# Kernel tuning notes

Hardware: AMD Instinct MI355X
Metric: run time of the kernel (lower is better)

## Reference

```python
import jax, jax.numpy as jnp
import numpy as np

B, V, S = 16, 100000, 4096
LOSS_WEIGHT = 1.0


def setup_inputs() -> dict:
    key = jax.random.key(0)
    k1, k2, k3, k4 = jax.random.split(key, 4)
    return {
        "src_verts": jax.random.normal(k1, (B, V, 3), dtype=jnp.float32),
        "dst_verts": jax.random.normal(k2, (B, V, 3), dtype=jnp.float32),
        "src_idx": jax.random.randint(k3, (B, S), 0, V, dtype=jnp.int64),
        "dst_idx": jax.random.randint(k4, (B, S), 0, V, dtype=jnp.int64),
    }


def _gather(verts, idx):
    # verts: (B, V, 3), idx: (B, S) -> (B, S, 3)
    return jnp.take_along_axis(verts, idx[:, :, None], axis=1)


def reference(src_verts, dst_verts, src_idx, dst_idx):
    src = _gather(src_verts, src_idx)  # (B, S, 3)
    dst = _gather(dst_verts, dst_idx)  # (B, S, 3)
    # squared euclidean distance matrix, matching torch.cdist(p=2)**2
    s2 = jnp.sum(src * src, axis=-1)  # (B, S)
    d2 = jnp.sum(dst * dst, axis=-1)  # (B, S)
    gram = jnp.einsum("bsc,btc->bst", src, dst)  # (B, S, S)
    dist_mat = jnp.maximum(s2[:, :, None] + d2[:, None, :] - 2.0 * gram, 0.0)
    # min over src points (dim=1) + min over dst points (dim=2)
    chamfer_distance = jnp.min(dist_mat, axis=1) + jnp.min(dist_mat, axis=2)  # (B, S)
    chamfer_loss = jnp.mean(chamfer_distance, axis=-1)  # (B,)
    chamfer_loss = jnp.mean(chamfer_loss, axis=0)  # scalar ('mean' reduction)
    return chamfer_loss * LOSS_WEIGHT
```

## Files before the change

kernel.cpp:

```cpp
#include <hip/hip_runtime.h>
#include <hip/hip_bf16.h>
#include <math.h>

#define B 16
#define V 100000
#define S 4096
#define BS (B * S)
#define NT 256
#define ONE_BF 0x3F80u

typedef __attribute__((ext_vector_type(8))) short bf16x8;
typedef __attribute__((ext_vector_type(16))) float f32x16;

static __device__ __forceinline__ unsigned bft(float x) {
  return __float_as_uint(x) >> 16;
}
static __device__ __forceinline__ float bff(unsigned hbits) {
  return __uint_as_float(hbits << 16);
}
static __device__ __forceinline__ unsigned pk(unsigned lo, unsigned hi) {
  return (lo & 0xFFFFu) | (hi << 16);
}
static __device__ __forceinline__ float min3(float a, float b, float c) {
  return fminf(fminf(a, b), c);
}


__global__ __launch_bounds__(256) void chamfer_prep_kernel(
    const float* __restrict__ src_verts, const float* __restrict__ dst_verts,
    const int* __restrict__ src_idx, const int* __restrict__ dst_idx,
    uint4* __restrict__ srcfrag, uint4* __restrict__ dstfrag,
    float* __restrict__ out) {
  int t = blockIdx.x * 256 + threadIdx.x;
  if (t == 0) *out = 0.f;
  int set = t >> 16;
  int i = t & (BS - 1);
  int b = i >> 12;

  const int* idx = set ? dst_idx : src_idx;
  const float* verts = set ? dst_verts : src_verts;
  int v = idx[i];
  v = v < 0 ? 0 : (v >= V ? V - 1 : v);
  const float* pv = verts + ((size_t)b * V + v) * 3;
  float x = pv[0], y = pv[1], z = pv[2];
  unsigned hx = bft(x), hy = bft(y), hz = bft(z);
  float n2 = x * x + y * y + z * z;
  unsigned n2h = bft(n2);
  unsigned n2l = bft(n2 - bff(n2h));

  if (set == 0) {
    unsigned lx = bft(x - bff(hx)), ly = bft(y - bff(hy)), lz = bft(z - bff(hz));
    int tile = i >> 5, c = i & 31;
    uint4* base = srcfrag + (size_t)tile * 64;
    base[c]      = make_uint4(pk(hx, hy), pk(hz, lx), pk(ly, lz), pk(hx, hy));
    base[32 + c] = make_uint4(pk(hz, n2h), pk(n2l, ONE_BF), pk(ONE_BF, 0u), 0u);
  } else {
    unsigned mx = bft(-2.f * bff(hx)), my = bft(-2.f * bff(hy)), mz = bft(-2.f * bff(hz));
    unsigned nx = bft(-2.f * (x - bff(hx)));
    unsigned ny = bft(-2.f * (y - bff(hy)));
    unsigned nz = bft(-2.f * (z - bff(hz)));
    dstfrag[(size_t)i * 2]     = make_uint4(pk(mx, my), pk(mz, mx), pk(my, mz), pk(nx, ny));
    dstfrag[(size_t)i * 2 + 1] = make_uint4(pk(nz, ONE_BF), pk(ONE_BF, n2h), pk(n2l, 0u), 0u);
  }
}

__global__ __launch_bounds__(NT, 2) void chamfer_mfma_kernel(
    const uint4* __restrict__ srcfrag, const uint4* __restrict__ dstfrag,
    float* __restrict__ part_src, float* __restrict__ part_dst) {
  __shared__ struct {
    uint4 sfrag[2048];
    unsigned smin[1024];
  } sh;
  float* red = (float*)sh.sfrag;

  int bid = blockIdx.x;
  int b = bid >> 6;
  int jp = (bid >> 2) & 15;
  int iq = bid & 3;
  int tid = threadIdx.x;

  const uint4* chunk = srcfrag + (size_t)(b * 128 + iq * 32) * 64;
  #pragma unroll
  for (int k = 0; k < 8; ++k) {
    sh.sfrag[tid + k * NT] = chunk[tid + k * NT];
  }
  #pragma unroll
  for (int k = 0; k < 4; ++k) sh.smin[tid + k * NT] = 0x7F800000u;

  int w = tid >> 6;
  int lane = tid & 63;
  int c = lane & 31, h = lane >> 5;
  int gj = b * S + jp * 256 + w * 64 + c;
  bf16x8 A0 = __builtin_bit_cast(bf16x8, dstfrag[(size_t)gj * 2 + h]);
  bf16x8 A1 = __builtin_bit_cast(bf16x8, dstfrag[(size_t)(gj + 32) * 2 + h]);

  __syncthreads();

  f32x16 zero = {};
  f32x16 mn0, mn1;
  #pragma unroll
  for (int r = 0; r < 16; ++r) { mn0[r] = INFINITY; mn1[r] = INFINITY; }

  int t0r = 8 * w;

  #define FOLD(dp0, dp1, tp)                                                 \
    {                                                                        \
      _Pragma("unroll")                                                      \
      for (int r = 0; r < 16; ++r) mn0[r] = fminf(mn0[r], dp0[r]);           \
      _Pragma("unroll")                                                      \
      for (int r = 0; r < 16; ++r) mn1[r] = fminf(mn1[r], dp1[r]);           \
      float t0 = min3(dp0[0], dp0[1], dp0[2]);                               \
      float t1 = min3(dp0[3], dp0[4], dp0[5]);                               \
      float t2 = min3(dp0[6], dp0[7], dp0[8]);                               \
      float t3 = min3(dp0[9], dp0[10], dp0[11]);                             \
      float t4 = min3(dp0[12], dp0[13], dp0[14]);                            \
      float u0 = min3(t0, t1, t2);                                           \
      float u1 = min3(t3, t4, dp0[15]);                                      \
      float s0 = min3(dp1[0], dp1[1], dp1[2]);                               \
      float s1 = min3(dp1[3], dp1[4], dp1[5]);                               \
      float s2 = min3(dp1[6], dp1[7], dp1[8]);                               \
      float s3 = min3(dp1[9], dp1[10], dp1[11]);                             \
      float s4 = min3(dp1[12], dp1[13], dp1[14]);                            \
      float v0 = min3(s0, s1, s2);                                           \
      float v1 = min3(s3, s4, dp1[15]);                                      \
      float m = fminf(min3(u0, u1, v0), v1);                                 \
      atomicMin(&sh.smin[(tp) * 32 + c], __float_as_uint(fmaxf(m, 0.f)));    \
    }

  int tprev = t0r & 31;
  bf16x8 Bf0 = __builtin_bit_cast(bf16x8, sh.sfrag[tprev * 64 + lane]);
  f32x16 dp0 = __builtin_amdgcn_mfma_f32_32x32x16_bf16(A0, Bf0, zero, 0, 0, 0);
  f32x16 dp1 = __builtin_amdgcn_mfma_f32_32x32x16_bf16(A1, Bf0, zero, 0, 0, 0);

  #pragma unroll 4
  for (int it = 1; it < 32; ++it) {
    int t = (it + t0r) & 31;
    bf16x8 Bc = __builtin_bit_cast(bf16x8, sh.sfrag[t * 64 + lane]);
    f32x16 dc0 = __builtin_amdgcn_mfma_f32_32x32x16_bf16(A0, Bc, zero, 0, 0, 0);
    f32x16 dc1 = __builtin_amdgcn_mfma_f32_32x32x16_bf16(A1, Bc, zero, 0, 0, 0);
    FOLD(dp0, dp1, tprev);
    dp0 = dc0;
    dp1 = dc1;
    tprev = t;
  }
  FOLD(dp0, dp1, tprev);
  #undef FOLD

  __syncthreads();
  #pragma unroll
  for (int k = 0; k < 4; ++k) {
    int p = tid + k * NT;
    part_src[jp * BS + b * S + iq * 1024 + p] = __uint_as_float(sh.smin[p]);
  }
  __syncthreads();

  #pragma unroll
  for (int r = 0; r < 16; ++r) {
    int row = w * 64 + (r & 3) + 8 * (r >> 2) + 4 * h;
    red[row * 33 + c] = mn0[r];
    red[(row + 32) * 33 + c] = mn1[r];
  }
  __syncthreads();
  {
    int row = tid;
    const float* rp = red + row * 33;
    float a0 = min3(rp[0], rp[1], rp[2]);
    float a1 = min3(rp[3], rp[4], rp[5]);
    float a2 = min3(rp[6], rp[7], rp[8]);
    float a3 = min3(rp[9], rp[10], rp[11]);
    float a4 = min3(rp[12], rp[13], rp[14]);
    float a5 = min3(rp[15], rp[16], rp[17]);
    float a6 = min3(rp[18], rp[19], rp[20]);
    float a7 = min3(rp[21], rp[22], rp[23]);
    float a8 = min3(rp[24], rp[25], rp[26]);
    float a9 = min3(rp[27], rp[28], rp[29]);
    float aa = fminf(rp[30], rp[31]);
    float b0 = min3(a0, a1, a2);
    float b1 = min3(a3, a4, a5);
    float b2 = min3(a6, a7, a8);
    float b3 = min3(a9, aa, b0);
    float m = min3(b1, b2, b3);
    part_dst[iq * BS + b * S + jp * 256 + row] = fmaxf(m, 0.f);
  }
}

__global__ __launch_bounds__(256) void chamfer_reduce_kernel(
    const float* __restrict__ parts, float* __restrict__ out) {
  __shared__ float red[4];
  int tid = threadIdx.x;
  const float4* ps = (const float4*)parts;
  const float4* pd = (const float4*)(parts + 16 * BS);

  float v = 0.f;
  int t4 = blockIdx.x * 256 + tid;
  if (t4 < BS / 4) {
    float4 ms = ps[t4];
    #pragma unroll
    for (int j = 1; j < 16; ++j) {
      float4 t = ps[j * (BS / 4) + t4];
      ms.x = fminf(ms.x, t.x); ms.y = fminf(ms.y, t.y);
      ms.z = fminf(ms.z, t.z); ms.w = fminf(ms.w, t.w);
    }
    float4 md = pd[t4];
    #pragma unroll
    for (int j = 1; j < 4; ++j) {
      float4 t = pd[j * (BS / 4) + t4];
      md.x = fminf(md.x, t.x); md.y = fminf(md.y, t.y);
      md.z = fminf(md.z, t.z); md.w = fminf(md.w, t.w);
    }
    v = (ms.x + ms.y + ms.z + ms.w) + (md.x + md.y + md.z + md.w);
    v *= (1.0f / (float)BS);
  }

  #pragma unroll
  for (int off = 32; off > 0; off >>= 1) v += __shfl_down(v, off, 64);
  if ((tid & 63) == 0) red[tid >> 6] = v;
  __syncthreads();
  if (tid == 0) atomicAdd(out, (red[0] + red[1]) + (red[2] + red[3]));
}

extern "C" void kernel_launch(void* const* d_in, const int* in_sizes, int n_in,
                              void* d_out, int out_size, void* d_ws, size_t ws_size,
                              hipStream_t stream) {
  const float* src_verts = (const float*)d_in[0];
  const float* dst_verts = (const float*)d_in[1];
  const int* src_idx = (const int*)d_in[2];
  const int* dst_idx = (const int*)d_in[3];
  float* out = (float*)d_out;

  float* parts = (float*)d_ws;
  float* part_src = parts;
  float* part_dst = parts + 16 * BS;
  uint4* srcfrag = (uint4*)(parts + 21 * BS);
  uint4* dstfrag = (uint4*)(parts + 29 * BS);

  chamfer_prep_kernel<<<2 * BS / 256, 256, 0, stream>>>(
      src_verts, dst_verts, src_idx, dst_idx, srcfrag, dstfrag, out);

  chamfer_mfma_kernel<<<B * 16 * 4, NT, 0, stream>>>(
      srcfrag, dstfrag, part_src, part_dst);

  chamfer_reduce_kernel<<<64, 256, 0, stream>>>(parts, out);
}
```

Before: 28.73 us.

## Fuse final reduction into MFMA kernel via last-blocks atomic barrier

Removes the separate reduce kernel launch. MFMA blocks take a completion ticket with an atomic counter, and the last 64 blocks to finish spin-wait until every block has written its partial minima, then run the min-and-sum reduction. This saves one kernel launch and its inter-kernel gap. In exchange it adds a global spin barrier and threadfences, and it depends on the last 64 finishers staying resident while the others complete.

```diff
diff --git a/kernel.cpp b/kernel.cpp
--- a/kernel.cpp
+++ b/kernel.cpp
@@ -7,6 +7,8 @@
 #define S 4096
 #define BS (B * S)
 #define NT 256
+#define GRID 1024
+#define NFIN 64
 #define ONE_BF 0x3F80u
 
 typedef __attribute__((ext_vector_type(8))) short bf16x8;
@@ -30,9 +32,13 @@
     const float* __restrict__ src_verts, const float* __restrict__ dst_verts,
     const int* __restrict__ src_idx, const int* __restrict__ dst_idx,
     uint4* __restrict__ srcfrag, uint4* __restrict__ dstfrag,
-    float* __restrict__ out) {
+    unsigned* __restrict__ sync2, float* __restrict__ out) {
   int t = blockIdx.x * 256 + threadIdx.x;
-  if (t == 0) *out = 0.f;
+  if (t == 0) {
+    *out = 0.f;
+    sync2[0] = 0u;
+    sync2[1] = 0u;
+  }
   int set = t >> 16;
   int i = t & (BS - 1);
   int b = i >> 12;
@@ -66,7 +72,8 @@
 
 __global__ __launch_bounds__(NT, 2) void chamfer_mfma_kernel(
     const uint4* __restrict__ srcfrag, const uint4* __restrict__ dstfrag,
-    float* __restrict__ part_src, float* __restrict__ part_dst) {
+    float* __restrict__ part_src, float* __restrict__ part_dst,
+    unsigned* __restrict__ sync2, float* __restrict__ out) {
   __shared__ struct {
     uint4 sfrag[2048];
     unsigned smin[1024];
@@ -182,41 +189,53 @@
     float m = min3(b1, b2, b3);
     part_dst[iq * BS + b * S + jp * 256 + row] = fmaxf(m, 0.f);
   }
-}
-
-__global__ __launch_bounds__(256) void chamfer_reduce_kernel(
-    const float* __restrict__ parts, float* __restrict__ out) {
-  __shared__ float red[4];
-  int tid = threadIdx.x;
-  const float4* ps = (const float4*)parts;
-  const float4* pd = (const float4*)(parts + 16 * BS);
-
-  float v = 0.f;
-  int t4 = blockIdx.x * 256 + tid;
-  if (t4 < BS / 4) {
-    float4 ms = ps[t4];
+
+  __threadfence();
+  __shared__ unsigned rank_sh;
+  if (tid == 0) rank_sh = atomicAdd(&sync2[0], 1u);
+  __syncthreads();
+  unsigned rank = rank_sh;
+  if (rank < GRID - NFIN) return;
+
+  if (rank == GRID - 1) {
+    __threadfence();
+    atomicExch(&sync2[1], 1u);
+  }
+  if (tid == 0) {
+    while (atomicAdd(&sync2[1], 0u) == 0u) { }
+  }
+  __syncthreads();
+
+  {
+    int slice = rank - (GRID - NFIN);
+    int i4 = slice * NT + tid;
+    const float4* ps = (const float4*)part_src;
+    const float4* pd = (const float4*)part_dst;
+
+    float4 ms = ps[i4];
     #pragma unroll
     for (int j = 1; j < 16; ++j) {
-      float4 t = ps[j * (BS / 4) + t4];
+      float4 t = ps[j * (BS / 4) + i4];
       ms.x = fminf(ms.x, t.x); ms.y = fminf(ms.y, t.y);
       ms.z = fminf(ms.z, t.z); ms.w = fminf(ms.w, t.w);
     }
-    float4 md = pd[t4];
+    float4 md = pd[i4];
     #pragma unroll
     for (int j = 1; j < 4; ++j) {
-      float4 t = pd[j * (BS / 4) + t4];
+      float4 t = pd[j * (BS / 4) + i4];
       md.x = fminf(md.x, t.x); md.y = fminf(md.y, t.y);
       md.z = fminf(md.z, t.z); md.w = fminf(md.w, t.w);
     }
-    v = (ms.x + ms.y + ms.z + ms.w) + (md.x + md.y + md.z + md.w);
+    float v = (ms.x + ms.y + ms.z + ms.w) + (md.x + md.y + md.z + md.w);
     v *= (1.0f / (float)BS);
-  }
-
-  #pragma unroll
-  for (int off = 32; off > 0; off >>= 1) v += __shfl_down(v, off, 64);
-  if ((tid & 63) == 0) red[tid >> 6] = v;
-  __syncthreads();
-  if (tid == 0) atomicAdd(out, (red[0] + red[1]) + (red[2] + red[3]));
+
+    #pragma unroll
+    for (int off = 32; off > 0; off >>= 1) v += __shfl_down(v, off, 64);
+    __shared__ float fred[4];
+    if ((tid & 63) == 0) fred[tid >> 6] = v;
+    __syncthreads();
+    if (tid == 0) atomicAdd(out, (fred[0] + fred[1]) + (fred[2] + fred[3]));
+  }
 }
 
 extern "C" void kernel_launch(void* const* d_in, const int* in_sizes, int n_in,
@@ -231,14 +250,13 @@
   float* parts = (float*)d_ws;
   float* part_src = parts;
   float* part_dst = parts + 16 * BS;
+  unsigned* sync2 = (unsigned*)(parts + 20 * BS);
   uint4* srcfrag = (uint4*)(parts + 21 * BS);
   uint4* dstfrag = (uint4*)(parts + 29 * BS);
 
   chamfer_prep_kernel<<<2 * BS / 256, 256, 0, stream>>>(
-      src_verts, dst_verts, src_idx, dst_idx, srcfrag, dstfrag, out);
-
-  chamfer_mfma_kernel<<<B * 16 * 4, NT, 0, stream>>>(
-      srcfrag, dstfrag, part_src, part_dst);
-
-  chamfer_reduce_kernel<<<64, 256, 0, stream>>>(parts, out);
-}
+      src_verts, dst_verts, src_idx, dst_idx, srcfrag, dstfrag, sync2, out);
+
+  chamfer_mfma_kernel<<<GRID, NT, 0, stream>>>(
+      srcfrag, dstfrag, part_src, part_dst, sync2, out);
+}
```

Result: slower. 105.6 us (+267.4%).
